# Kernel tuning notes

Hardware: AMD Instinct MI355X
Metric: run time of the kernel (lower is better)

Reference implementation:

```python
import jax, jax.numpy as jnp
import numpy as np

N_EXPERTS = 8
TOP_K = 2

# NOTE: dropout is treated as identity (inference/eval mode), matching
# nn.Dropout in eval(). gate_logits returned is post-softmax, exactly as in
# the torch code (it overwrites gate_logits with F.softmax output).

def setup_inputs() -> dict:
    key = jax.random.key(0)
    k1, k2, k3, k4 = jax.random.split(key, 4)
    B, T, S = 32, 512, 512
    x = jax.random.normal(k1, (B, T, S), dtype=jnp.float32)
    gate_w = jax.random.normal(k2, (N_EXPERTS, S), dtype=jnp.float32) * (1.0 / np.sqrt(S))
    expert_w = jax.random.normal(k3, (N_EXPERTS, S, S), dtype=jnp.float32) * (1.0 / np.sqrt(S))
    expert_b = jax.random.normal(k4, (N_EXPERTS, S), dtype=jnp.float32) * 0.01
    return {"x": x, "gate_w": gate_w, "expert_w": expert_w, "expert_b": expert_b}


def reference(x, gate_w, expert_w, expert_b):
    # Gating: Linear(seq_len -> n_experts, no bias) then softmax over experts
    logits = jnp.einsum('bti,ei->bte', x, gate_w)          # [B,T,E]
    gates = jax.nn.softmax(logits, axis=-1)                # [B,T,E]
    # top-k routing weights
    w, sel = jax.lax.top_k(gates, TOP_K)                   # [B,T,K], [B,T,K]
    # dense combine weights: zero except at selected experts
    comb = jnp.sum(jax.nn.one_hot(sel, N_EXPERTS, dtype=x.dtype) * w[..., None], axis=-2)  # [B,T,E]
    # all-expert linear outputs (XLA fuses the weighted combine)
    expert_out = jnp.einsum('bti,eoi->bteo', x, expert_w) + expert_b[None, None]  # [B,T,E,S]
    out = jnp.einsum('bte,bteo->bto', comb, expert_out)    # [B,T,S]
    out = jax.nn.relu(out)
    return (out, gates)
```

## Files before the change

kernel.cpp:

```cpp
#include <hip/hip_runtime.h>
#include <stdint.h>

#define NT 16384
#define SDIM 512
#define NE 8
#define BM 64
#define BN 128
#define BK 32
#define NSTEP (SDIM / BK)
#define NPAIR 28
#define MAX_TILES 284
#define GEMM_GRID (MAX_TILES * 4)

typedef __attribute__((ext_vector_type(8))) short short8v;
typedef __attribute__((ext_vector_type(8))) unsigned short ushort8v;
typedef __attribute__((ext_vector_type(4))) float f32x4;

#define GLOAD_LDS16(gp, lp) __builtin_amdgcn_global_load_lds( \
    (const __attribute__((address_space(1))) uint32_t*)(gp), \
    (__attribute__((address_space(3))) uint32_t*)(lp), 16, 0, 0)

__device__ __forceinline__ unsigned short f2bf(float f) {
  uint32_t x = __float_as_uint(f);
  x = (x + 0x7FFFu + ((x >> 16) & 1u)) >> 16;
  return (unsigned short)x;
}

__global__ __launch_bounds__(256) void gate_conv_kernel(
    const float* __restrict__ x, const float* __restrict__ gw,
    const float* __restrict__ ew,
    unsigned short* __restrict__ xb, unsigned short* __restrict__ wb,
    float* __restrict__ gates_out, float* __restrict__ wts,
    int* __restrict__ sels, int* __restrict__ cnt) {
  if (blockIdx.x == 0 && threadIdx.x < 32) cnt[threadIdx.x] = 0;

  int lane = threadIdx.x & 63;
  int wv = threadIdx.x >> 6;

  float4 ga[NE], gb[NE];
#pragma unroll
  for (int e = 0; e < NE; e++) {
    const float4* g4 = (const float4*)(gw + e * SDIM + lane * 8);
    ga[e] = g4[0]; gb[e] = g4[1];
  }

  int tbase = blockIdx.x * 16 + wv * 4;
#pragma unroll 1
  for (int i = 0; i < 4; i++) {
    int t = tbase + i;
    const float* xr = x + (size_t)t * SDIM;
    float4 xa = ((const float4*)xr)[lane * 2];
    float4 xbv = ((const float4*)xr)[lane * 2 + 1];

    ushort8v u;
    u[0] = f2bf(xa.x); u[1] = f2bf(xa.y); u[2] = f2bf(xa.z); u[3] = f2bf(xa.w);
    u[4] = f2bf(xbv.x); u[5] = f2bf(xbv.y); u[6] = f2bf(xbv.z); u[7] = f2bf(xbv.w);
    *(ushort8v*)(xb + (size_t)t * SDIM + lane * 8) = u;

    double part[NE];
#pragma unroll
    for (int e = 0; e < NE; e++) {
      double s;
      s  = (double)xa.x * ga[e].x;  s += (double)xa.y * ga[e].y;
      s += (double)xa.z * ga[e].z;  s += (double)xa.w * ga[e].w;
      s += (double)xbv.x * gb[e].x; s += (double)xbv.y * gb[e].y;
      s += (double)xbv.z * gb[e].z; s += (double)xbv.w * gb[e].w;
      part[e] = s;
    }
#pragma unroll
    for (int e = 0; e < NE; e++) {
#pragma unroll
      for (int off = 32; off >= 1; off >>= 1)
        part[e] += __shfl_xor(part[e], off, 64);
    }

    float lg[NE];
#pragma unroll
    for (int e = 0; e < NE; e++) lg[e] = (float)part[e];
    float mx = lg[0];
#pragma unroll
    for (int e = 1; e < NE; e++) mx = fmaxf(mx, lg[e]);
    float ex[NE]; float sum = 0.f;
#pragma unroll
    for (int e = 0; e < NE; e++) { ex[e] = expf(lg[e] - mx); sum += ex[e]; }
    float inv = 1.0f / sum;
    float g[NE];
#pragma unroll
    for (int e = 0; e < NE; e++) g[e] = ex[e] * inv;

    int s0 = 0; float v0 = g[0];
#pragma unroll
    for (int e = 1; e < NE; e++) if (g[e] > v0) { v0 = g[e]; s0 = e; }
    int s1 = -1; float v1 = -1.0f;
#pragma unroll
    for (int e = 0; e < NE; e++) if (e != s0 && g[e] > v1) { v1 = g[e]; s1 = e; }

    if (lane == 0) {
      float* go = gates_out + (size_t)t * NE;
#pragma unroll
      for (int e = 0; e < NE; e++) go[e] = g[e];
      wts[t * 2] = v0; wts[t * 2 + 1] = v1;
      sels[t * 2] = s0; sels[t * 2 + 1] = s1;
    }
  }

  int ci = (blockIdx.x * 256 + threadIdx.x) * 8;
  const float4* p = (const float4*)(ew + ci);
  float4 a = p[0], b = p[1];
  ushort8v w;
  w[0] = f2bf(a.x); w[1] = f2bf(a.y); w[2] = f2bf(a.z); w[3] = f2bf(a.w);
  w[4] = f2bf(b.x); w[5] = f2bf(b.y); w[6] = f2bf(b.z); w[7] = f2bf(b.w);
  *(ushort8v*)(wb + ci) = w;
}

__global__ __launch_bounds__(1024) void scatter_kernel(
    const int* __restrict__ sels, int* __restrict__ cnt, int* __restrict__ list) {
  __shared__ int lc[NPAIR];
  __shared__ int lb[NPAIR];
  int tid = threadIdx.x;
  if (tid < NPAIR) lc[tid] = 0;
  __syncthreads();
  int t = blockIdx.x * 1024 + tid;
  int s0 = sels[t * 2], s1 = sels[t * 2 + 1];
  int a = min(s0, s1), b = max(s0, s1);
  int tri = 7 * a - ((a * (a - 1)) >> 1) + (b - a - 1);
  int p = atomicAdd(&lc[tri], 1);
  __syncthreads();
  if (tid < NPAIR) lb[tid] = atomicAdd(cnt + tid, lc[tid]);
  __syncthreads();
  list[tri * NT + lb[tri] + p] = t;
}

__global__ void build_tiles(const int* __restrict__ cnt, int4* __restrict__ desc) {
  int lane = threadIdx.x & 63;
  int c = (lane < NPAIR) ? cnt[lane] : 0;
  int nt = (c + BM - 1) / BM;
  int pre = nt;
#pragma unroll
  for (int off = 1; off < 32; off <<= 1) {
    int v = __shfl_up(pre, off, 64);
    if (lane >= off) pre += v;
  }
  pre -= nt;
  int total = __shfl(pre + nt, NPAIR - 1, 64);
  if (lane < NPAIR) {
    int a = 0, rem = lane;
    while (rem >= 7 - a) { rem -= 7 - a; a++; }
    int b = a + 1 + rem;
    int k = 0;
    for (int s = 0; s < c; s += BM, k++)
      desc[pre + k] = make_int4(a | (b << 8) | (lane << 16), s, min(BM, c - s), 0);
  }
  for (int j = total + lane; j < MAX_TILES; j += 64)
    desc[j] = make_int4(0, 0, 0, 0);
}

__global__ __launch_bounds__(256, 4) void moe_gemm(
    const unsigned short* __restrict__ xb, const unsigned short* __restrict__ wbuf,
    const int* __restrict__ list, const float* __restrict__ wts,
    const int* __restrict__ sels, const int4* __restrict__ desc,
    const float* __restrict__ ebias, float* __restrict__ out) {
  int flat = blockIdx.x;
  int v = (flat & 7) * (GEMM_GRID / 8) + (flat >> 3);
  int tile = v >> 2, nb = v & 3;

  int4 d = desc[tile];
  int rows = d.z;
  if (rows == 0) return;
  int ea = d.x & 255, eb2 = (d.x >> 8) & 255, tri = d.x >> 16;
  int start = d.y;
  int nbase = nb * BN;
  const int* gl = list + tri * NT + start;

  __shared__ unsigned short lA[2][BM * BK];
  __shared__ unsigned short lB[2][2 * BN * BK];

  int tid = threadIdx.x, lane = tid & 63, wv = tid >> 6;

  int pa = tid >> 3, qa = tid & 7;
  int rowA = 2 * pa + (qa >> 2);
  int k16A = (qa & 3) ^ (pa & 3);
  int tokA = (rowA < rows) ? gl[rowA] : gl[0];
  const unsigned short* srcA = xb + (size_t)tokA * SDIM + k16A * 8;

  const unsigned short* srcB[4];
#pragma unroll
  for (int g = 0; g < 4; g++) {
    int c = g * 256 + tid;
    int slot = c >> 9;
    int cc = c & 511;
    int p = cc >> 3, q = cc & 7;
    int row = 2 * p + (q >> 2);
    int k16 = (q & 3) ^ (p & 3);
    int e = slot ? eb2 : ea;
    srcB[g] = wbuf + (size_t)(e * SDIM + nbase + row) * SDIM + k16 * 8;
  }

  char* lAb = (char*)lA;
  char* lBb = (char*)lB;
  int wm = wv >> 1, wn = wv & 1;
  int arow = wm * 32 + (lane & 15);
  int brow = wn * 64 + (lane & 15);
  int kreg = lane >> 4;

  int offA[2], offB[2][4];
#pragma unroll
  for (int mi = 0; mi < 2; mi++) {
    int lr = arow + mi * 16;
    int p = lr >> 1, h = lr & 1;
    offA[mi] = p * 128 + (h * 4 + (kreg ^ (p & 3))) * 16;
  }
#pragma unroll
  for (int s = 0; s < 2; s++)
#pragma unroll
    for (int ni = 0; ni < 4; ni++) {
      int lr = brow + ni * 16;
      int p = lr >> 1, h = lr & 1;
      offB[s][ni] = s * 8192 + p * 128 + (h * 4 + (kreg ^ (p & 3))) * 16;
    }

  f32x4 acc[2][2][4];
#pragma unroll
  for (int s = 0; s < 2; s++)
#pragma unroll
    for (int i = 0; i < 2; i++)
#pragma unroll
      for (int j = 0; j < 4; j++) acc[s][i][j] = (f32x4){0.f, 0.f, 0.f, 0.f};

#define STAGE(st, k0) do { \
    GLOAD_LDS16(srcA + (k0), lAb + (st) * 4096 + tid * 16); \
    _Pragma("unroll") \
    for (int g = 0; g < 4; g++) \
      GLOAD_LDS16(srcB[g] + (k0), lBb + (st) * 16384 + (g * 256 + tid) * 16); \
  } while (0)

#define COMPUTE(st) do { \
    const char* pA = lAb + (st) * 4096; \
    const char* pB = lBb + (st) * 16384; \
    short8v a[2]; \
    _Pragma("unroll") \
    for (int mi = 0; mi < 2; mi++) a[mi] = *(const short8v*)(pA + offA[mi]); \
    _Pragma("unroll") \
    for (int s = 0; s < 2; s++) { \
      short8v b[4]; \
      _Pragma("unroll") \
      for (int ni = 0; ni < 4; ni++) b[ni] = *(const short8v*)(pB + offB[s][ni]); \
      _Pragma("unroll") \
      for (int mi = 0; mi < 2; mi++) \
        _Pragma("unroll") \
        for (int ni = 0; ni < 4; ni++) \
          acc[s][mi][ni] = __builtin_amdgcn_mfma_f32_16x16x32_bf16(a[mi], b[ni], acc[s][mi][ni], 0, 0, 0); \
    } \
  } while (0)

  STAGE(0, 0);
#pragma unroll 1
  for (int t = 0; t < NSTEP; t++) {
    if (t + 1 < NSTEP) {
      STAGE((t + 1) & 1, (t + 1) * BK);
      asm volatile("s_waitcnt vmcnt(5)" ::: "memory");
    } else {
      asm volatile("s_waitcnt vmcnt(0)" ::: "memory");
    }
    __builtin_amdgcn_s_barrier();
    __builtin_amdgcn_sched_barrier(0);
    __builtin_amdgcn_s_setprio(1);
    COMPUTE(t & 1);
    __builtin_amdgcn_s_setprio(0);
    __builtin_amdgcn_s_barrier();
  }

  int rg = lane >> 4;
  int ncol = nbase + wn * 64 + (lane & 15);
  float bA[4], bB[4];
#pragma unroll
  for (int ni = 0; ni < 4; ni++) {
    bA[ni] = ebias[ea * SDIM + ncol + ni * 16];
    bB[ni] = ebias[eb2 * SDIM + ncol + ni * 16];
  }
#pragma unroll
  for (int mi = 0; mi < 2; mi++) {
#pragma unroll
    for (int r = 0; r < 4; r++) {
      int m = wm * 32 + mi * 16 + rg * 4 + r;
      if (m < rows) {
        int tok = gl[m];
        float2 wp = *(const float2*)&wts[tok * 2];
        int sA = sels[tok * 2];
        float wA = (sA == ea) ? wp.x : wp.y;
        float wB = (sA == ea) ? wp.y : wp.x;
        float* orow = out + (size_t)tok * SDIM + ncol;
#pragma unroll
        for (int ni = 0; ni < 4; ni++) {
          float vv = wA * (acc[0][mi][ni][r] + bA[ni]) + wB * (acc[1][mi][ni][r] + bB[ni]);
          orow[ni * 16] = fmaxf(vv, 0.f);
        }
      }
    }
  }
#undef STAGE
#undef COMPUTE
}

extern "C" void kernel_launch(void* const* d_in, const int* in_sizes, int n_in,
                              void* d_out, int out_size, void* d_ws, size_t ws_size,
                              hipStream_t stream) {
  const float* x        = (const float*)d_in[0];
  const float* gate_w   = (const float*)d_in[1];
  const float* expert_w = (const float*)d_in[2];
  const float* expert_b = (const float*)d_in[3];
  float* out = (float*)d_out;

  char* ws = (char*)d_ws;
  unsigned short* xb = (unsigned short*)(ws);
  unsigned short* wb = (unsigned short*)(ws + 16777216);
  float* wts  = (float*)(ws + 20971520);
  int* sels   = (int*)(ws + 21102592);
  int* cnt    = (int*)(ws + 21233664);
  int* list   = (int*)(ws + 21233792);
  int4* desc  = (int4*)(ws + 23068800);

  gate_conv_kernel<<<NT / 16, 256, 0, stream>>>(x, gate_w, expert_w, xb, wb,
                                                out + (size_t)NT * SDIM,
                                                wts, sels, cnt);
  scatter_kernel<<<NT / 1024, 1024, 0, stream>>>(sels, cnt, list);
  build_tiles<<<1, 64, 0, stream>>>(cnt, desc);
  moe_gemm<<<GEMM_GRID, 256, 0, stream>>>(xb, wb, list, wts, sels, desc,
                                          expert_b, out);
}
```

Before: 75.09 us.

## Drop build_tiles launch, compute tile descriptors in-kernel, halve BN

```diff
diff --git a/kernel.cpp b/kernel.cpp
--- a/kernel.cpp
+++ b/kernel.cpp
@@ -5,12 +5,12 @@
 #define SDIM 512
 #define NE 8
 #define BM 64
-#define BN 128
+#define BN 64
 #define BK 32
 #define NSTEP (SDIM / BK)
 #define NPAIR 28
-#define MAX_TILES 284
-#define GEMM_GRID (MAX_TILES * 4)
+#define MAX_TILES 283
+#define GEMM_GRID (MAX_TILES * 8)
 
 typedef __attribute__((ext_vector_type(8))) short short8v;
 typedef __attribute__((ext_vector_type(8))) unsigned short ushort8v;
@@ -131,44 +131,33 @@
   list[tri * NT + lb[tri] + p] = t;
 }
 
-__global__ void build_tiles(const int* __restrict__ cnt, int4* __restrict__ desc) {
-  int lane = threadIdx.x & 63;
-  int c = (lane < NPAIR) ? cnt[lane] : 0;
-  int nt = (c + BM - 1) / BM;
-  int pre = nt;
-#pragma unroll
-  for (int off = 1; off < 32; off <<= 1) {
-    int v = __shfl_up(pre, off, 64);
-    if (lane >= off) pre += v;
-  }
-  pre -= nt;
-  int total = __shfl(pre + nt, NPAIR - 1, 64);
-  if (lane < NPAIR) {
-    int a = 0, rem = lane;
-    while (rem >= 7 - a) { rem -= 7 - a; a++; }
-    int b = a + 1 + rem;
-    int k = 0;
-    for (int s = 0; s < c; s += BM, k++)
-      desc[pre + k] = make_int4(a | (b << 8) | (lane << 16), s, min(BM, c - s), 0);
-  }
-  for (int j = total + lane; j < MAX_TILES; j += 64)
-    desc[j] = make_int4(0, 0, 0, 0);
-}
-
 __global__ __launch_bounds__(256, 4) void moe_gemm(
     const unsigned short* __restrict__ xb, const unsigned short* __restrict__ wbuf,
     const int* __restrict__ list, const float* __restrict__ wts,
-    const int* __restrict__ sels, const int4* __restrict__ desc,
+    const int* __restrict__ sels, const int* __restrict__ cnt,
     const float* __restrict__ ebias, float* __restrict__ out) {
   int flat = blockIdx.x;
-  int v = (flat & 7) * (GEMM_GRID / 8) + (flat >> 3);
-  int tile = v >> 2, nb = v & 3;
-
-  int4 d = desc[tile];
-  int rows = d.z;
-  if (rows == 0) return;
-  int ea = d.x & 255, eb2 = (d.x >> 8) & 255, tri = d.x >> 16;
-  int start = d.y;
+  int v = (flat & 7) * MAX_TILES + (flat >> 3);
+  int tileIdx = v >> 3, nb = v & 7;
+
+  int tri = -1, start = 0, rows = 0, ea = 0, eb2 = 0;
+  {
+    int pre = 0, a = 0, b = 1;
+#pragma unroll 1
+    for (int t = 0; t < NPAIR; t++) {
+      int c = cnt[t];
+      int nt = (c + BM - 1) / BM;
+      if (tileIdx < pre + nt) {
+        tri = t; start = (tileIdx - pre) * BM; rows = min(BM, c - start);
+        ea = a; eb2 = b;
+        break;
+      }
+      pre += nt;
+      b++; if (b == NE) { a++; b = a + 1; }
+    }
+  }
+  if (tri < 0) return;
+
   int nbase = nb * BN;
   const int* gl = list + tri * NT + start;
 
@@ -183,12 +172,12 @@
   int tokA = (rowA < rows) ? gl[rowA] : gl[0];
   const unsigned short* srcA = xb + (size_t)tokA * SDIM + k16A * 8;
 
-  const unsigned short* srcB[4];
-#pragma unroll
-  for (int g = 0; g < 4; g++) {
+  const unsigned short* srcB[2];
+#pragma unroll
+  for (int g = 0; g < 2; g++) {
     int c = g * 256 + tid;
-    int slot = c >> 9;
-    int cc = c & 511;
+    int slot = c >> 8;
+    int cc = c & 255;
     int p = cc >> 3, q = cc & 7;
     int row = 2 * p + (q >> 2);
     int k16 = (q & 3) ^ (p & 3);
@@ -200,10 +189,10 @@
   char* lBb = (char*)lB;
   int wm = wv >> 1, wn = wv & 1;
   int arow = wm * 32 + (lane & 15);
-  int brow = wn * 64 + (lane & 15);
+  int brow = wn * 32 + (lane & 15);
   int kreg = lane >> 4;
 
-  int offA[2], offB[2][4];
+  int offA[2], offB[2][2];
 #pragma unroll
   for (int mi = 0; mi < 2; mi++) {
     int lr = arow + mi * 16;
@@ -213,42 +202,42 @@
 #pragma unroll
   for (int s = 0; s < 2; s++)
 #pragma unroll
-    for (int ni = 0; ni < 4; ni++) {
+    for (int ni = 0; ni < 2; ni++) {
       int lr = brow + ni * 16;
       int p = lr >> 1, h = lr & 1;
-      offB[s][ni] = s * 8192 + p * 128 + (h * 4 + (kreg ^ (p & 3))) * 16;
-    }
-
-  f32x4 acc[2][2][4];
+      offB[s][ni] = s * 4096 + p * 128 + (h * 4 + (kreg ^ (p & 3))) * 16;
+    }
+
+  f32x4 acc[2][2][2];
 #pragma unroll
   for (int s = 0; s < 2; s++)
 #pragma unroll
     for (int i = 0; i < 2; i++)
 #pragma unroll
-      for (int j = 0; j < 4; j++) acc[s][i][j] = (f32x4){0.f, 0.f, 0.f, 0.f};
+      for (int j = 0; j < 2; j++) acc[s][i][j] = (f32x4){0.f, 0.f, 0.f, 0.f};
 
 #define STAGE(st, k0) do { \
     GLOAD_LDS16(srcA + (k0), lAb + (st) * 4096 + tid * 16); \
     _Pragma("unroll") \
-    for (int g = 0; g < 4; g++) \
-      GLOAD_LDS16(srcB[g] + (k0), lBb + (st) * 16384 + (g * 256 + tid) * 16); \
+    for (int g = 0; g < 2; g++) \
+      GLOAD_LDS16(srcB[g] + (k0), lBb + (st) * 8192 + (g * 256 + tid) * 16); \
   } while (0)
 
 #define COMPUTE(st) do { \
     const char* pA = lAb + (st) * 4096; \
-    const char* pB = lBb + (st) * 16384; \
+    const char* pB = lBb + (st) * 8192; \
     short8v a[2]; \
     _Pragma("unroll") \
     for (int mi = 0; mi < 2; mi++) a[mi] = *(const short8v*)(pA + offA[mi]); \
     _Pragma("unroll") \
     for (int s = 0; s < 2; s++) { \
-      short8v b[4]; \
+      short8v b[2]; \
       _Pragma("unroll") \
-      for (int ni = 0; ni < 4; ni++) b[ni] = *(const short8v*)(pB + offB[s][ni]); \
+      for (int ni = 0; ni < 2; ni++) b[ni] = *(const short8v*)(pB + offB[s][ni]); \
       _Pragma("unroll") \
       for (int mi = 0; mi < 2; mi++) \
         _Pragma("unroll") \
-        for (int ni = 0; ni < 4; ni++) \
+        for (int ni = 0; ni < 2; ni++) \
           acc[s][mi][ni] = __builtin_amdgcn_mfma_f32_16x16x32_bf16(a[mi], b[ni], acc[s][mi][ni], 0, 0, 0); \
     } \
   } while (0)
@@ -258,7 +247,7 @@
   for (int t = 0; t < NSTEP; t++) {
     if (t + 1 < NSTEP) {
       STAGE((t + 1) & 1, (t + 1) * BK);
-      asm volatile("s_waitcnt vmcnt(5)" ::: "memory");
+      asm volatile("s_waitcnt vmcnt(3)" ::: "memory");
     } else {
       asm volatile("s_waitcnt vmcnt(0)" ::: "memory");
     }
@@ -271,10 +260,10 @@
   }
 
   int rg = lane >> 4;
-  int ncol = nbase + wn * 64 + (lane & 15);
-  float bA[4], bB[4];
-#pragma unroll
-  for (int ni = 0; ni < 4; ni++) {
+  int ncol = nbase + wn * 32 + (lane & 15);
+  float bA[2], bB[2];
+#pragma unroll
+  for (int ni = 0; ni < 2; ni++) {
     bA[ni] = ebias[ea * SDIM + ncol + ni * 16];
     bB[ni] = ebias[eb2 * SDIM + ncol + ni * 16];
   }
@@ -291,7 +280,7 @@
         float wB = (sA == ea) ? wp.y : wp.x;
         float* orow = out + (size_t)tok * SDIM + ncol;
 #pragma unroll
-        for (int ni = 0; ni < 4; ni++) {
+        for (int ni = 0; ni < 2; ni++) {
           float vv = wA * (acc[0][mi][ni][r] + bA[ni]) + wB * (acc[1][mi][ni][r] + bB[ni]);
           orow[ni * 16] = fmaxf(vv, 0.f);
         }
@@ -318,13 +307,11 @@
   int* sels   = (int*)(ws + 21102592);
   int* cnt    = (int*)(ws + 21233664);
   int* list   = (int*)(ws + 21233792);
-  int4* desc  = (int4*)(ws + 23068800);
 
   gate_conv_kernel<<<NT / 16, 256, 0, stream>>>(x, gate_w, expert_w, xb, wb,
                                                 out + (size_t)NT * SDIM,
                                                 wts, sels, cnt);
   scatter_kernel<<<NT / 1024, 1024, 0, stream>>>(sels, cnt, list);
-  build_tiles<<<1, 64, 0, stream>>>(cnt, desc);
-  moe_gemm<<<GEMM_GRID, 256, 0, stream>>>(xb, wb, list, wts, sels, desc,
+  moe_gemm<<<GEMM_GRID, 256, 0, stream>>>(xb, wb, list, wts, sels, cnt,
                                           expert_b, out);
 }
```

Result: no change. 75.90 us (+1.1%).
